# Optimization experiments

Measured on AMD Instinct MI355X. Metric: run time of the kernel, lower is better.

The kernel has to match this reference:

```python
import jax, jax.numpy as jnp
import numpy as np

EPS = 1e-5

def _ln(x, g, b):
    mu = jnp.mean(x, axis=-1, keepdims=True)
    var = jnp.mean(jnp.square(x - mu), axis=-1, keepdims=True)
    return (x - mu) * jax.lax.rsqrt(var + EPS) * g + b

def _lrelu(x):
    return jnp.where(x >= 0, x, 0.1 * x)  # LeakyReLU(0.1)

def _layer(x, w, b, g, be, act):
    # PointLinearLayer: Linear -> LayerNorm -> (optional) LeakyReLU(0.1)
    y = _ln(jnp.matmul(x, w) + b, g, be)
    return _lrelu(y) if act else y

def setup_inputs():
    key = jax.random.key(0)
    ks = jax.random.split(key, 16)
    B, Ns, Nd, K, Cin, Cout, PE, M = 1, 10000, 40000, 16, 128, 128, 32, 16
    w = lambda k, i, o: jax.random.normal(k, (i, o), jnp.float32) * 0.02
    z = lambda n: jnp.zeros((n,), jnp.float32)
    o = lambda n: jnp.ones((n,), jnp.float32)
    return {
        "sparse_xyz": jax.random.normal(ks[0], (B, Ns, 3), jnp.float32),
        "sparse_feats": jax.random.normal(ks[1], (B, Ns, Cin), jnp.float32),
        "nei_inds": jax.random.randint(ks[2], (B, Nd, K), 0, Ns),
        "sparse_xyz_norm": jax.random.normal(ks[3], (B, Ns, 3), jnp.float32),
        "dense_xyz": jax.random.normal(ks[4], (B, Nd, 3), jnp.float32),
        "dense_xyz_norm": jax.random.normal(ks[5], (B, Nd, 3), jnp.float32),
        "dense_feats": jax.random.normal(ks[6], (B, Nd, Cout), jnp.float32),
        # pe_convs WeightNet(3 -> 32, hidden=[32]): L0 3->32 LN+act, L1 32->32 LN
        "pe_w0": w(ks[7], 3, PE), "pe_b0": z(PE), "pe_g0": o(PE), "pe_be0": z(PE),
        "pe_w1": w(ks[8], PE, PE), "pe_b1": z(PE), "pe_g1": o(PE), "pe_be1": z(PE),
        # main WeightNet(3 -> 16, hidden=[16,16]): L0,L1 LN+act, L2 LN
        "wn_w0": w(ks[9], 3, M), "wn_b0": z(M), "wn_g0": o(M), "wn_be0": z(M),
        "wn_w1": w(ks[10], M, M), "wn_b1": z(M), "wn_g1": o(M), "wn_be1": z(M),
        "wn_w2": w(ks[11], M, M), "wn_b2": z(M), "wn_g2": o(M), "wn_be2": z(M),
        # final PointLinearLayer: (Cin+PE)*M -> Cout with LN + LeakyReLU(0.1)
        "lin_w": w(ks[12], (Cin + PE) * M, Cout), "lin_b": z(Cout),
        "lin_g": o(Cout), "lin_be": z(Cout),
    }

def reference(sparse_xyz, sparse_feats, nei_inds, sparse_xyz_norm, dense_xyz,
              dense_xyz_norm, dense_feats,
              pe_w0, pe_b0, pe_g0, pe_be0, pe_w1, pe_b1, pe_g1, pe_be1,
              wn_w0, wn_b0, wn_g0, wn_be0, wn_w1, wn_b1, wn_g1, wn_be1,
              wn_w2, wn_b2, wn_g2, wn_be2, lin_w, lin_b, lin_g, lin_be):
    gather = jax.vmap(lambda t, i: t[i])  # per-batch kNN gather
    loc = gather(sparse_xyz, nei_inds) - dense_xyz[:, :, None, :]   # B,Nd,K,3 relative coords (weightNetInput, USE_VI=False)
    g_feat = gather(sparse_feats, nei_inds)                          # B,Nd,K,Cin
    # positional-encoding WeightNet on relative coords (USE_PE)
    pe = _layer(loc, pe_w0, pe_b0, pe_g0, pe_be0, True)
    pe = _layer(pe, pe_w1, pe_b1, pe_g1, pe_be1, False)              # B,Nd,K,32
    feat = jnp.concatenate([g_feat, pe], axis=-1)                    # B,Nd,K,Cin+32
    # main WeightNet generates per-neighbor mixing weights
    wts = _layer(loc, wn_w0, wn_b0, wn_g0, wn_be0, True)
    wts = _layer(wts, wn_w1, wn_b1, wn_g1, wn_be1, True)
    wts = _layer(wts, wn_w2, wn_b2, wn_g2, wn_be2, False)            # B,Nd,K,16
    B, Nd = nei_inds.shape[:2]
    # matmul(feat^T, wts) over K, flatten channel x mid dims (C-major, matches torch .view)
    out = jnp.einsum('bnkc,bnkm->bncm', feat, wts).reshape(B, Nd, -1)
    out = _layer(out, lin_w, lin_b, lin_g, lin_be, True)             # B,Nd,Cout
    return out + dense_feats                                         # shortcut dense features
```

## Files before the change

kernel.cpp:

```cpp
#include <hip/hip_runtime.h>

#define NPB  16
#define KNN  16
#define CIN  128
#define CF   160
#define MM   16
#define PEC  32
#define COUT 128
#define KDIM 2560
#define FRE  768
#define LEPS 1e-5f

typedef __bf16 bf16x8 __attribute__((ext_vector_type(8)));
typedef float  f32x4  __attribute__((ext_vector_type(4)));
union U16x8 { uint4 u4; bf16x8 b; unsigned short us[8]; };

#define SW_PE_W0   0
#define SW_PE_B0   96
#define SW_PE_G0   128
#define SW_PE_BE0  160
#define SW_PE_W1   192
#define SW_PE_B1   1216
#define SW_PE_G1   1248
#define SW_PE_BE1  1280
#define SW_WN_W0   1312
#define SW_WN_B0   1360
#define SW_WN_G0   1376
#define SW_WN_BE0  1392
#define SW_WN_W1   1408
#define SW_WN_B1   1664
#define SW_WN_G1   1680
#define SW_WN_BE1  1696
#define SW_WN_W2   1712
#define SW_WN_B2   1968
#define SW_WN_G2   1984
#define SW_WN_BE2  2000
#define SW_TOTAL   2016

__device__ __forceinline__ float bf2f(unsigned short b){
  union { unsigned int u; float f; } x; x.u = ((unsigned int)b) << 16; return x.f;
}
__device__ __forceinline__ unsigned short f2bf(float f){
  union { float f; unsigned int u; } x; x.f = f;
  unsigned int r = (x.u + 0x7fffu + ((x.u >> 16) & 1u)) >> 16;
  return (unsigned short)r;
}
__device__ __forceinline__ unsigned short f2b(float f){
  union { __bf16 h; unsigned short u; } v; v.h = (__bf16)f; return v.u;
}
__device__ __forceinline__ float rsum16(float v){
  v += __shfl_xor(v, 8, 16);
  v += __shfl_xor(v, 4, 16);
  v += __shfl_xor(v, 2, 16);
  v += __shfl_xor(v, 1, 16);
  return v;
}
__device__ __forceinline__ float rsum32(float v){
  v += __shfl_xor(v, 16, 32);
  v += __shfl_xor(v, 8, 32);
  v += __shfl_xor(v, 4, 32);
  v += __shfl_xor(v, 2, 32);
  v += __shfl_xor(v, 1, 32);
  return v;
}
__device__ __forceinline__ float lrelu(float v){ return v >= 0.f ? v : 0.1f * v; }

template<int N>
__device__ __forceinline__ void ln_inlane(float* v, const float* g, const float* be, bool act){
  float mu = 0.f;
#pragma unroll
  for (int i = 0; i < N; ++i) mu += v[i];
  mu *= (1.f / N);
  float var = 0.f;
#pragma unroll
  for (int i = 0; i < N; ++i) { float d = v[i] - mu; var += d * d; }
  const float rs = rsqrtf(var * (1.f / N) + LEPS);
#pragma unroll
  for (int i = 0; i < N; ++i) {
    float y = (v[i] - mu) * rs * g[i] + be[i];
    v[i] = act ? lrelu(y) : y;
  }
}

__global__ __launch_bounds__(256)
void pct_prep(const float* __restrict__ lin_w, unsigned short* __restrict__ wpack,
              const float* __restrict__ sf, unsigned short* __restrict__ sfb16,
              const int n4)
{
  const int bid = blockIdx.x;
  if (bid < 160) {
    const int u    = bid * 256 + threadIdx.x;
    const int lane = u & 63;
    const int tt   = (u >> 6) & 7;
    const int s    = u >> 9;
    const int ipb  = s * 32 + ((lane >> 4) * 8);
    const int nn   = tt * 16 + (lane & 15);
    unsigned short v[8];
#pragma unroll
    for (int j = 0; j < 8; ++j) {
      const int ip  = ipb + j;
      const int r   = ip & 3;
      const int ctl = (ip >> 2) & 1;
      const int qq  = (ip >> 3) & 3;
      const int c16 = (ip >> 5) & 15;
      const int P   = ip >> 9;
      const int c   = P * 32 + ctl * 16 + c16;
      const int m   = qq * 4 + r;
      v[j] = f2bf(lin_w[(long)(c * MM + m) * COUT + nn]);
    }
    *(uint4*)(wpack + (long)u * 8) = *(uint4*)v;
  } else {
    const int i = (bid - 160) * 256 + threadIdx.x;
    if (i >= n4) return;
    const float4 v = ((const float4*)sf)[i];
    union { unsigned short us[4]; uint2 u; } r;
    r.us[0] = f2b(v.x); r.us[1] = f2b(v.y); r.us[2] = f2b(v.z); r.us[3] = f2b(v.w);
    ((uint2*)sfb16)[i] = r.u;
  }
}

__global__ __launch_bounds__(256)
void pct_nets(
    const float* __restrict__ sparse_xyz,
    const int* __restrict__ nei_inds,
    const float* __restrict__ dense_xyz,
    const float* __restrict__ pe_w0, const float* __restrict__ pe_b0,
    const float* __restrict__ pe_g0, const float* __restrict__ pe_be0,
    const float* __restrict__ pe_w1, const float* __restrict__ pe_b1,
    const float* __restrict__ pe_g1, const float* __restrict__ pe_be1,
    const float* __restrict__ wn_w0, const float* __restrict__ wn_b0,
    const float* __restrict__ wn_g0, const float* __restrict__ wn_be0,
    const float* __restrict__ wn_w1, const float* __restrict__ wn_b1,
    const float* __restrict__ wn_g1, const float* __restrict__ wn_be1,
    const float* __restrict__ wn_w2, const float* __restrict__ wn_b2,
    const float* __restrict__ wn_g2, const float* __restrict__ wn_be2,
    unsigned short* __restrict__ fragw)
{
  __shared__ float sw[SW_TOTAL];
  __shared__ __align__(16) unsigned short wtsf[16 * 256];
  __shared__ __align__(16) unsigned short pef[16 * 512];

  const int t     = threadIdx.x;
  const int nbase = blockIdx.x * NPB;

  for (int i = t; i < 96;   i += 256) sw[SW_PE_W0 + i] = pe_w0[i];
  for (int i = t; i < 32;   i += 256) {
    sw[SW_PE_B0 + i] = pe_b0[i];  sw[SW_PE_G0 + i] = pe_g0[i];  sw[SW_PE_BE0 + i] = pe_be0[i];
    sw[SW_PE_B1 + i] = pe_b1[i];  sw[SW_PE_G1 + i] = pe_g1[i];  sw[SW_PE_BE1 + i] = pe_be1[i];
  }
  for (int i = t; i < 1024; i += 256) sw[SW_PE_W1 + i] = pe_w1[i];
  for (int i = t; i < 48;   i += 256) sw[SW_WN_W0 + i] = wn_w0[i];
  for (int i = t; i < 16;   i += 256) {
    sw[SW_WN_B0 + i] = wn_b0[i];  sw[SW_WN_G0 + i] = wn_g0[i];  sw[SW_WN_BE0 + i] = wn_be0[i];
    sw[SW_WN_B1 + i] = wn_b1[i];  sw[SW_WN_G1 + i] = wn_g1[i];  sw[SW_WN_BE1 + i] = wn_be1[i];
    sw[SW_WN_B2 + i] = wn_b2[i];  sw[SW_WN_G2 + i] = wn_g2[i];  sw[SW_WN_BE2 + i] = wn_be2[i];
  }
  for (int i = t; i < 256;  i += 256) { sw[SW_WN_W1 + i] = wn_w1[i]; sw[SW_WN_W2 + i] = wn_w2[i]; }
  __syncthreads();

  {
    const int p  = t >> 4;
    const int kk = t & 15;
    const int n  = nbase + p;
    const int idx = nei_inds[n * KNN + kk];
    const float x0 = sparse_xyz[idx*3+0] - dense_xyz[n*3+0];
    const float x1 = sparse_xyz[idx*3+1] - dense_xyz[n*3+1];
    const float x2 = sparse_xyz[idx*3+2] - dense_xyz[n*3+2];

    float h[32];
#pragma unroll
    for (int c = 0; c < 32; ++c)
      h[c] = x0*sw[SW_PE_W0+c] + x1*sw[SW_PE_W0+32+c] + x2*sw[SW_PE_W0+64+c] + sw[SW_PE_B0+c];
    ln_inlane<32>(h, &sw[SW_PE_G0], &sw[SW_PE_BE0], true);

    float z[32];
#pragma unroll
    for (int c = 0; c < 32; ++c) z[c] = sw[SW_PE_B1 + c];
#pragma unroll 4
    for (int j = 0; j < 32; ++j) {
      const float hj = h[j];
#pragma unroll
      for (int c = 0; c < 32; ++c) z[c] += hj * sw[SW_PE_W1 + j*32 + c];
    }
    ln_inlane<32>(z, &sw[SW_PE_G1], &sw[SW_PE_BE1], false);
    {
      union { unsigned short us[32]; uint4 u4[4]; } zb;
#pragma unroll
      for (int c = 0; c < 32; ++c) zb.us[c] = f2b(z[c]);
      unsigned short* pp_ = pef + p*512 + kk*32;
#pragma unroll
      for (int j = 0; j < 4; ++j) *(uint4*)(pp_ + j*8) = zb.u4[j];
    }

    float w[16];
#pragma unroll
    for (int m = 0; m < 16; ++m)
      w[m] = x0*sw[SW_WN_W0+m] + x1*sw[SW_WN_W0+16+m] + x2*sw[SW_WN_W0+32+m] + sw[SW_WN_B0+m];
    ln_inlane<16>(w, &sw[SW_WN_G0], &sw[SW_WN_BE0], true);

    float z2[16];
#pragma unroll
    for (int m = 0; m < 16; ++m) z2[m] = sw[SW_WN_B1 + m];
#pragma unroll 4
    for (int j = 0; j < 16; ++j) {
      const float wj = w[j];
#pragma unroll
      for (int m = 0; m < 16; ++m) z2[m] += wj * sw[SW_WN_W1 + j*16 + m];
    }
    ln_inlane<16>(z2, &sw[SW_WN_G1], &sw[SW_WN_BE1], true);

#pragma unroll
    for (int m = 0; m < 16; ++m) w[m] = sw[SW_WN_B2 + m];
#pragma unroll 4
    for (int j = 0; j < 16; ++j) {
      const float wj = z2[j];
#pragma unroll
      for (int m = 0; m < 16; ++m) w[m] += wj * sw[SW_WN_W2 + j*16 + m];
    }
    ln_inlane<16>(w, &sw[SW_WN_G2], &sw[SW_WN_BE2], false);
    {
      unsigned short* wf = wtsf + p*256 + ((kk >> 3) << 7) + (kk & 7);
#pragma unroll
      for (int m = 0; m < 16; ++m) wf[m*8] = f2b(w[m]);
    }
  }

  {
    const int lane = t & 63;
    const int wave = t >> 6;
    const int l2   = lane & 31;
    const int ct2  = lane >> 5;
#pragma unroll
    for (int i = 0; i < 4; ++i) {
      const int p = wave*4 + i;
      unsigned short* fw = fragw + (size_t)(nbase + p) * FRE;
      if (lane < 32) {
        const uint4 a = *(const uint4*)(wtsf + p*256 + lane*8);
        *(uint4*)(fw + lane*8) = a;
      }
      union { unsigned short us[8]; uint4 u4; } o;
#pragma unroll
      for (int j = 0; j < 8; ++j)
        o.us[j] = pef[p*512 + ((l2 >> 4)*8 + j)*32 + ct2*16 + (l2 & 15)];
      *(uint4*)(fw + 256 + ct2*256 + l2*8) = o.u4;
    }
  }
}

__global__ __launch_bounds__(256)
void pct_eg(
    const int* __restrict__ nei_inds,
    const unsigned short* __restrict__ sfb16,
    const unsigned short* __restrict__ fragw,
    const unsigned short* __restrict__ wpack,
    const float* __restrict__ lin_b, const float* __restrict__ lin_g,
    const float* __restrict__ lin_be, const float* __restrict__ dense_feats,
    float* __restrict__ out)
{
  __shared__ __align__(16) union FU {
    unsigned short feats[16][2048];
    float outs[16][132];
  } fu;
  __shared__ __align__(16) unsigned short aL[16][512];

  const int t     = threadIdx.x;
  const int nbase = blockIdx.x * NPB;
  const int lane  = t & 63;
  const int wave  = t >> 6;
  const int q     = lane >> 4;
  const int mq    = lane & 15;

  int idxall[4][4];
#pragma unroll
  for (int i = 0; i < 4; ++i)
#pragma unroll
    for (int t4 = 0; t4 < 4; ++t4)
      idxall[i][t4] = nei_inds[(nbase + wave*4 + i) * KNN + t4*4 + q];

  U16x8 af[4], pe0[4], pe1[4];
  const uint4 zero4 = {0u, 0u, 0u, 0u};
#pragma unroll
  for (int i = 0; i < 4; ++i) {
    const int p = wave*4 + i;
#pragma unroll
    for (int t4 = 0; t4 < 4; ++t4)
      __builtin_amdgcn_global_load_lds(
          (const void*)(sfb16 + (size_t)idxall[i][t4] * CIN + mq * 8),
          (void*)((char*)fu.feats[p] + t4 * 1024), 16, 0, 0);
    const unsigned short* fw = fragw + (size_t)(nbase + p) * FRE;
    af[i].u4  = (lane < 32) ? *(const uint4*)(fw + lane*8) : zero4;
    pe0[i].u4 = *(const uint4*)(fw + 256 + (lane & 31)*8);
    pe1[i].u4 = *(const uint4*)(fw + 512 + (lane & 31)*8);
  }
  __syncthreads();

  f32x4 acc0 = {0.f,0.f,0.f,0.f}, acc1 = {0.f,0.f,0.f,0.f};
  const unsigned short* wpl = wpack + ((size_t)(wave*2) * 64 + lane) * 8;

#pragma unroll 1
  for (int P = 0; P < 5; ++P) {
#pragma unroll
    for (int i = 0; i < 4; ++i) {
      const int p = wave*4 + i;
      f32x4 a0 = {0.f,0.f,0.f,0.f}, a1 = {0.f,0.f,0.f,0.f};
      if (P < 4) {
        const unsigned short* sb = &fu.feats[p][0] + (q & 1) * 1024 + mq;
        U16x8 b0_, b1_;
#pragma unroll
        for (int j = 0; j < 8; ++j) b0_.us[j] = sb[j * CIN + (2*P    ) * 16];
#pragma unroll
        for (int j = 0; j < 8; ++j) b1_.us[j] = sb[j * CIN + (2*P + 1) * 16];
        a0 = __builtin_amdgcn_mfma_f32_16x16x32_bf16(af[i].b, b0_.b, a0, 0, 0, 0);
        a1 = __builtin_amdgcn_mfma_f32_16x16x32_bf16(af[i].b, b1_.b, a1, 0, 0, 0);
      } else {
        a0 = __builtin_amdgcn_mfma_f32_16x16x32_bf16(af[i].b, pe0[i].b, a0, 0, 0, 0);
        a1 = __builtin_amdgcn_mfma_f32_16x16x32_bf16(af[i].b, pe1[i].b, a1, 0, 0, 0);
      }
      union { unsigned short us[8]; uint4 u4; } o;
#pragma unroll
      for (int r = 0; r < 4; ++r) { o.us[r] = f2b(a0[r]); o.us[4+r] = f2b(a1[r]); }
      *(uint4*)((char*)aL[p] + ((mq*64 + q*16) ^ ((p & 7) << 4))) = o.u4;
    }
    __syncthreads();

#pragma unroll
    for (int s = 0; s < 16; ++s) {
      const int sg = P*16 + s;
      U16x8 af2;
      af2.u4 = *(const uint4*)((char*)aL[mq] + ((s*64 + q*16) ^ ((mq & 7) << 4)));
      const unsigned short* wpb = wpl + (size_t)sg * 4096;
      U16x8 b0_, b1_;
      b0_.u4 = *(const uint4*)(wpb);
      b1_.u4 = *(const uint4*)(wpb + 512);
      acc0 = __builtin_amdgcn_mfma_f32_16x16x32_bf16(af2.b, b0_.b, acc0, 0, 0, 0);
      acc1 = __builtin_amdgcn_mfma_f32_16x16x32_bf16(af2.b, b1_.b, acc1, 0, 0, 0);
    }
    __syncthreads();
  }

#pragma unroll
  for (int r = 0; r < 4; ++r) {
    fu.outs[q*4 + r][(wave*2    )*16 + mq] = acc0[r];
    fu.outs[q*4 + r][(wave*2 + 1)*16 + mq] = acc1[r];
  }
  __syncthreads();

  {
    const int p   = t >> 4;
    const int l16 = t & 15;
    const int n   = nbase + p;
    float v[8];
#pragma unroll
    for (int i = 0; i < 2; ++i) {
      const int cb = (i*16 + l16) * 4;
      const float4 r  = *(const float4*)(&fu.outs[p][cb]);
      const float4 bb = *(const float4*)(lin_b + cb);
      v[i*4+0] = r.x + bb.x; v[i*4+1] = r.y + bb.y;
      v[i*4+2] = r.z + bb.z; v[i*4+3] = r.w + bb.w;
    }
    float sum = 0.f;
#pragma unroll
    for (int i = 0; i < 8; ++i) sum += v[i];
    const float mu = rsum16(sum) * (1.f/128.f);
    float qs = 0.f;
#pragma unroll
    for (int i = 0; i < 8; ++i) { float d = v[i] - mu; qs += d*d; }
    const float rs = rsqrtf(rsum16(qs) * (1.f/128.f) + LEPS);
#pragma unroll
    for (int i = 0; i < 2; ++i) {
      const int cb = (i*16 + l16) * 4;
      const float4 g  = *(const float4*)(lin_g  + cb);
      const float4 be = *(const float4*)(lin_be + cb);
      const float4 df = *(const float4*)(dense_feats + (long)n*COUT + cb);
      float4 y;
      y.x = lrelu((v[i*4+0]-mu)*rs*g.x + be.x) + df.x;
      y.y = lrelu((v[i*4+1]-mu)*rs*g.y + be.y) + df.y;
      y.z = lrelu((v[i*4+2]-mu)*rs*g.z + be.z) + df.z;
      y.w = lrelu((v[i*4+3]-mu)*rs*g.w + be.w) + df.w;
      *(float4*)(out + (long)n*COUT + cb) = y;
    }
  }
}

__global__ __launch_bounds__(256)
void pct_fused(
    const float* __restrict__ sparse_xyz,
    const float* __restrict__ sparse_feats,
    const int* __restrict__ nei_inds,
    const float* __restrict__ dense_xyz,
    const float* __restrict__ dense_feats,
    const float* __restrict__ pe_w0, const float* __restrict__ pe_b0,
    const float* __restrict__ pe_g0, const float* __restrict__ pe_be0,
    const float* __restrict__ pe_w1, const float* __restrict__ pe_b1,
    const float* __restrict__ pe_g1, const float* __restrict__ pe_be1,
    const float* __restrict__ wn_w0, const float* __restrict__ wn_b0,
    const float* __restrict__ wn_g0, const float* __restrict__ wn_be0,
    const float* __restrict__ wn_w1, const float* __restrict__ wn_b1,
    const float* __restrict__ wn_g1, const float* __restrict__ wn_be1,
    const float* __restrict__ wn_w2, const float* __restrict__ wn_b2,
    const float* __restrict__ wn_g2, const float* __restrict__ wn_be2,
    const float* __restrict__ lin_w, const float* __restrict__ lin_b,
    const float* __restrict__ lin_g, const float* __restrict__ lin_be,
    float* __restrict__ out)
{
  __shared__ __align__(16) unsigned short feat_s[KNN][CF];
  __shared__ float wts_s[KNN][MM];
  __shared__ float loc_s[KNN][3];
  __shared__ int   nei_s[KNN];
  __shared__ __align__(16) unsigned short out_tile[CF*MM][8];

  const int t  = threadIdx.x;
  const int n0 = blockIdx.x * 8;
  const int k  = t >> 4;
  const int l  = t & 15;

#pragma unroll 1
  for (int p = 0; p < 8; ++p) {
    const int n = n0 + p;
    if (t < KNN) {
      int idx = nei_inds[n*KNN + t];
      nei_s[t] = idx;
      loc_s[t][0] = sparse_xyz[idx*3+0] - dense_xyz[n*3+0];
      loc_s[t][1] = sparse_xyz[idx*3+1] - dense_xyz[n*3+1];
      loc_s[t][2] = sparse_xyz[idx*3+2] - dense_xyz[n*3+2];
    }
    __syncthreads();
    {
      const int gk = t >> 4;
      const int c8 = (t & 15) * 8;
      const float* src = sparse_feats + (long)nei_s[gk]*CIN + c8;
      const float4 va = *(const float4*)(src);
      const float4 vb = *(const float4*)(src + 4);
      unsigned short* dst = &feat_s[gk][c8];
      dst[0] = f2bf(va.x); dst[1] = f2bf(va.y); dst[2] = f2bf(va.z); dst[3] = f2bf(va.w);
      dst[4] = f2bf(vb.x); dst[5] = f2bf(vb.y); dst[6] = f2bf(vb.z); dst[7] = f2bf(vb.w);
    }
    const float x0 = loc_s[k][0], x1 = loc_s[k][1], x2 = loc_s[k][2];
    const int c0 = l, c1 = l + 16;
    float ha = x0*pe_w0[0*PEC+c0] + x1*pe_w0[1*PEC+c0] + x2*pe_w0[2*PEC+c0] + pe_b0[c0];
    float hb = x0*pe_w0[0*PEC+c1] + x1*pe_w0[1*PEC+c1] + x2*pe_w0[2*PEC+c1] + pe_b0[c1];
    {
      float mu = rsum16(ha + hb) * (1.f/32.f);
      float da = ha - mu, db = hb - mu;
      float q  = rsum16(da*da + db*db);
      float rs = rsqrtf(q*(1.f/32.f) + LEPS);
      ha = lrelu(da*rs*pe_g0[c0] + pe_be0[c0]);
      hb = lrelu(db*rs*pe_g0[c1] + pe_be0[c1]);
    }
    float za = pe_b1[c0], zb = pe_b1[c1];
#pragma unroll
    for (int j = 0; j < 16; ++j) {
      float va = __shfl(ha, j, 16);
      float vb = __shfl(hb, j, 16);
      za += va * pe_w1[j*PEC + c0] + vb * pe_w1[(j+16)*PEC + c0];
      zb += va * pe_w1[j*PEC + c1] + vb * pe_w1[(j+16)*PEC + c1];
    }
    {
      float mu = rsum16(za + zb) * (1.f/32.f);
      float da = za - mu, db = zb - mu;
      float q  = rsum16(da*da + db*db);
      float rs = rsqrtf(q*(1.f/32.f) + LEPS);
      feat_s[k][CIN + c0] = f2bf(da*rs*pe_g1[c0] + pe_be1[c0]);
      feat_s[k][CIN + c1] = f2bf(db*rs*pe_g1[c1] + pe_be1[c1]);
    }
    float w0v = x0*wn_w0[0*MM+l] + x1*wn_w0[1*MM+l] + x2*wn_w0[2*MM+l] + wn_b0[l];
    {
      float mu = rsum16(w0v) * (1.f/16.f);
      float d  = w0v - mu;
      float rs = rsqrtf(rsum16(d*d)*(1.f/16.f) + LEPS);
      w0v = lrelu(d*rs*wn_g0[l] + wn_be0[l]);
    }
    float w1v = wn_b1[l];
#pragma unroll
    for (int j = 0; j < 16; ++j)
      w1v += __shfl(w0v, j, 16) * wn_w1[j*MM + l];
    {
      float mu = rsum16(w1v) * (1.f/16.f);
      float d  = w1v - mu;
      float rs = rsqrtf(rsum16(d*d)*(1.f/16.f) + LEPS);
      w1v = lrelu(d*rs*wn_g1[l] + wn_be1[l]);
    }
    float w2v = wn_b2[l];
#pragma unroll
    for (int j = 0; j < 16; ++j)
      w2v += __shfl(w1v, j, 16) * wn_w2[j*MM + l];
    {
      float mu = rsum16(w2v) * (1.f/16.f);
      float d  = w2v - mu;
      float rs = rsqrtf(rsum16(d*d)*(1.f/16.f) + LEPS);
      w2v = d*rs*wn_g2[l] + wn_be2[l];
    }
    wts_s[k][l] = w2v;
    __syncthreads();
    {
      const int m = t & 15;
      const int g = t >> 4;
      float wv[KNN];
#pragma unroll
      for (int kk = 0; kk < KNN; ++kk) wv[kk] = wts_s[kk][m];
#pragma unroll
      for (int j = 0; j < 10; ++j) {
        const int c = g*10 + j;
        float acc = 0.f;
#pragma unroll
        for (int kk = 0; kk < KNN; ++kk)
          acc += bf2f(feat_s[kk][c]) * wv[kk];
        out_tile[c*MM + m][p] = f2bf(acc);
      }
    }
    __syncthreads();
  }
  {
    const int h  = t >> 6;
    const int o0 = (t & 63) * 2;
    float acc0[8], acc1[8];
#pragma unroll
    for (int p = 0; p < 8; ++p) { acc0[p] = 0.f; acc1[p] = 0.f; }
    const int i0 = h * 640;
    for (int i = i0; i < i0 + 640; ++i) {
      const float2 wv = *(const float2*)(lin_w + (long)i*COUT + o0);
      const float wa = wv.x;
      const float wc = wv.y;
      const uint4 r = *(const uint4*)(&out_tile[i][0]);
      const float f0 = bf2f((unsigned short)(r.x & 0xffffu));
      const float f1 = bf2f((unsigned short)(r.x >> 16));
      const float g2 = bf2f((unsigned short)(r.y & 0xffffu));
      const float g3 = bf2f((unsigned short)(r.y >> 16));
      const float g4 = bf2f((unsigned short)(r.z & 0xffffu));
      const float g5 = bf2f((unsigned short)(r.z >> 16));
      const float g6 = bf2f((unsigned short)(r.w & 0xffffu));
      const float g7 = bf2f((unsigned short)(r.w >> 16));
      acc0[0] += f0*wa; acc1[0] += f0*wc;
      acc0[1] += f1*wa; acc1[1] += f1*wc;
      acc0[2] += g2*wa; acc1[2] += g2*wc;
      acc0[3] += g3*wa; acc1[3] += g3*wc;
      acc0[4] += g4*wa; acc1[4] += g4*wc;
      acc0[5] += g5*wa; acc1[5] += g5*wc;
      acc0[6] += g6*wa; acc1[6] += g6*wc;
      acc0[7] += g7*wa; acc1[7] += g7*wc;
    }
    __syncthreads();
    float* red = (float*)&out_tile[0][0];
#pragma unroll
    for (int p = 0; p < 8; ++p) {
      red[((h*8 + p) << 7) + o0    ] = acc0[p];
      red[((h*8 + p) << 7) + o0 + 1] = acc1[p];
    }
    __syncthreads();
    const int p2 = t >> 5, l2 = t & 31;
    const int n  = n0 + p2;
    float v[4];
#pragma unroll
    for (int j = 0; j < 4; ++j) {
      const int o = l2 + (j << 5);
      float sv = red[((0*8 + p2) << 7) + o] + red[((1*8 + p2) << 7) + o]
               + red[((2*8 + p2) << 7) + o] + red[((3*8 + p2) << 7) + o];
      v[j] = sv + lin_b[o];
    }
    float mu = rsum32(v[0] + v[1] + v[2] + v[3]) * (1.f/128.f);
    float q = 0.f;
#pragma unroll
    for (int j = 0; j < 4; ++j) { float d = v[j] - mu; q += d*d; }
    float rs = rsqrtf(rsum32(q) * (1.f/128.f) + LEPS);
#pragma unroll
    for (int j = 0; j < 4; ++j) {
      const int o = l2 + (j << 5);
      float y = (v[j] - mu) * rs * lin_g[o] + lin_be[o];
      y = lrelu(y);
      y += dense_feats[n*COUT + o];
      out[n*COUT + o] = y;
    }
  }
}

extern "C" void kernel_launch(void* const* d_in, const int* in_sizes, int n_in,
                              void* d_out, int out_size, void* d_ws, size_t ws_size,
                              hipStream_t stream) {
  const int Nd = in_sizes[2] / KNN;
  const int Ns = in_sizes[1] / CIN;
  const size_t fr_bytes = (size_t)Nd * FRE * 2;
  const size_t w_bytes  = (size_t)KDIM * COUT * 2;
  const size_t f_bytes  = (size_t)Ns * CIN * 2;
  const bool use_split = (ws_size >= fr_bytes + w_bytes + f_bytes)
                         && (Nd % NPB == 0) && ((Ns * CIN) % 4 == 0);

  if (use_split) {
    unsigned short* fragw = (unsigned short*)d_ws;
    unsigned short* wpack = (unsigned short*)((char*)d_ws + fr_bytes);
    unsigned short* sfb16 = (unsigned short*)((char*)d_ws + fr_bytes + w_bytes);

    const int n4 = Ns * CIN / 4;
    pct_prep<<<dim3(160 + (n4 + 255)/256), dim3(256), 0, stream>>>(
      (const float*)d_in[27], wpack, (const float*)d_in[1], sfb16, n4);

    pct_nets<<<dim3(Nd / NPB), dim3(256), 0, stream>>>(
      (const float*)d_in[0],  (const int*)d_in[2],  (const float*)d_in[4],
      (const float*)d_in[7],  (const float*)d_in[8],  (const float*)d_in[9],  (const float*)d_in[10],
      (const float*)d_in[11], (const float*)d_in[12], (const float*)d_in[13], (const float*)d_in[14],
      (const float*)d_in[15], (const float*)d_in[16], (const float*)d_in[17], (const float*)d_in[18],
      (const float*)d_in[19], (const float*)d_in[20], (const float*)d_in[21], (const float*)d_in[22],
      (const float*)d_in[23], (const float*)d_in[24], (const float*)d_in[25], (const float*)d_in[26],
      fragw);

    pct_eg<<<dim3(Nd / NPB), dim3(256), 0, stream>>>(
      (const int*)d_in[2], sfb16, fragw, wpack,
      (const float*)d_in[28], (const float*)d_in[29], (const float*)d_in[30],
      (const float*)d_in[6], (float*)d_out);
  } else {
    pct_fused<<<dim3(Nd / 8), dim3(256), 0, stream>>>(
      (const float*)d_in[0],  (const float*)d_in[1],  (const int*)d_in[2],
      (const float*)d_in[4],  (const float*)d_in[6],
      (const float*)d_in[7],  (const float*)d_in[8],  (const float*)d_in[9],  (const float*)d_in[10],
      (const float*)d_in[11], (const float*)d_in[12], (const float*)d_in[13], (const float*)d_in[14],
      (const float*)d_in[15], (const float*)d_in[16], (const float*)d_in[17], (const float*)d_in[18],
      (const float*)d_in[19], (const float*)d_in[20], (const float*)d_in[21], (const float*)d_in[22],
      (const float*)d_in[23], (const float*)d_in[24], (const float*)d_in[25], (const float*)d_in[26],
      (const float*)d_in[27], (const float*)d_in[28], (const float*)d_in[29], (const float*)d_in[30],
      (float*)d_out);
  }
}
```

Baseline: 284.1 us.

## Split gather-GEMM kernel across 8 waves and swizzle feature LDS layout

Doubles the block to 512 threads so each wave handles two points and a single 16-column output tile of the final linear layer. This halves per-wave register state and weight streaming. It also XOR-swizzles the gathered neighbor-feature rows in LDS so the strided column reads avoid bank conflicts. The epilogue LayerNorm is remapped to 32 threads per point. The cost is more waves contending for barriers and the same per-block LDS footprint.

After: 318.7 us. +12.2%, slower.

```diff
diff --git a/kernel.cpp b/kernel.cpp
--- a/kernel.cpp
+++ b/kernel.cpp
@@ -247,7 +247,7 @@
   }
 }
 
-__global__ __launch_bounds__(256)
+__global__ __launch_bounds__(512, 4)
 void pct_eg(
     const int* __restrict__ nei_inds,
     const unsigned short* __restrict__ sfb16,
@@ -269,23 +269,26 @@
   const int wave  = t >> 6;
   const int q     = lane >> 4;
   const int mq    = lane & 15;
-
-  int idxall[4][4];
-#pragma unroll
-  for (int i = 0; i < 4; ++i)
+  const int q1    = q & 1;
+  const int mqh   = mq >> 3, mql = mq & 7;
+
+  int idxall[2][4];
+#pragma unroll
+  for (int i = 0; i < 2; ++i)
 #pragma unroll
     for (int t4 = 0; t4 < 4; ++t4)
-      idxall[i][t4] = nei_inds[(nbase + wave*4 + i) * KNN + t4*4 + q];
-
-  U16x8 af[4], pe0[4], pe1[4];
+      idxall[i][t4] = nei_inds[(nbase + wave*2 + i) * KNN + t4*4 + q];
+
+  U16x8 af[2], pe0[2], pe1[2];
   const uint4 zero4 = {0u, 0u, 0u, 0u};
 #pragma unroll
-  for (int i = 0; i < 4; ++i) {
-    const int p = wave*4 + i;
+  for (int i = 0; i < 2; ++i) {
+    const int p = wave*2 + i;
 #pragma unroll
     for (int t4 = 0; t4 < 4; ++t4)
       __builtin_amdgcn_global_load_lds(
-          (const void*)(sfb16 + (size_t)idxall[i][t4] * CIN + mq * 8),
+          (const void*)(sfb16 + (size_t)idxall[i][t4] * CIN
+                        + ((mq ^ ((t4 >> 1) << 1)) * 8)),
           (void*)((char*)fu.feats[p] + t4 * 1024), 16, 0, 0);
     const unsigned short* fw = fragw + (size_t)(nbase + p) * FRE;
     af[i].u4  = (lane < 32) ? *(const uint4*)(fw + lane*8) : zero4;
@@ -294,22 +297,23 @@
   }
   __syncthreads();
 
-  f32x4 acc0 = {0.f,0.f,0.f,0.f}, acc1 = {0.f,0.f,0.f,0.f};
-  const unsigned short* wpl = wpack + ((size_t)(wave*2) * 64 + lane) * 8;
+  f32x4 acc = {0.f,0.f,0.f,0.f};
 
 #pragma unroll 1
   for (int P = 0; P < 5; ++P) {
 #pragma unroll
-    for (int i = 0; i < 4; ++i) {
-      const int p = wave*4 + i;
+    for (int i = 0; i < 2; ++i) {
+      const int p = wave*2 + i;
       f32x4 a0 = {0.f,0.f,0.f,0.f}, a1 = {0.f,0.f,0.f,0.f};
       if (P < 4) {
-        const unsigned short* sb = &fu.feats[p][0] + (q & 1) * 1024 + mq;
+        const int slot0 = (4*P     + mqh) ^ (q1 << 1);
+        const int slot1 = (4*P + 2 + mqh) ^ (q1 << 1);
+        const unsigned short* fb = &fu.feats[p][0] + q1*1024 + mql;
         U16x8 b0_, b1_;
 #pragma unroll
-        for (int j = 0; j < 8; ++j) b0_.us[j] = sb[j * CIN + (2*P    ) * 16];
-#pragma unroll
-        for (int j = 0; j < 8; ++j) b1_.us[j] = sb[j * CIN + (2*P + 1) * 16];
+        for (int j = 0; j < 8; ++j) b0_.us[j] = fb[j*128 + slot0*8];
+#pragma unroll
+        for (int j = 0; j < 8; ++j) b1_.us[j] = fb[j*128 + slot1*8];
         a0 = __builtin_amdgcn_mfma_f32_16x16x32_bf16(af[i].b, b0_.b, a0, 0, 0, 0);
         a1 = __builtin_amdgcn_mfma_f32_16x16x32_bf16(af[i].b, b1_.b, a1, 0, 0, 0);
       } else {
@@ -328,57 +332,40 @@
       const int sg = P*16 + s;
       U16x8 af2;
       af2.u4 = *(const uint4*)((char*)aL[mq] + ((s*64 + q*16) ^ ((mq & 7) << 4)));
-      const unsigned short* wpb = wpl + (size_t)sg * 4096;
-      U16x8 b0_, b1_;
-      b0_.u4 = *(const uint4*)(wpb);
-      b1_.u4 = *(const uint4*)(wpb + 512);
-      acc0 = __builtin_amdgcn_mfma_f32_16x16x32_bf16(af2.b, b0_.b, acc0, 0, 0, 0);
-      acc1 = __builtin_amdgcn_mfma_f32_16x16x32_bf16(af2.b, b1_.b, acc1, 0, 0, 0);
+      U16x8 b_;
+      b_.u4 = *(const uint4*)(wpack + ((size_t)(sg*8 + wave) * 64 + lane) * 8);
+      acc = __builtin_amdgcn_mfma_f32_16x16x32_bf16(af2.b, b_.b, acc, 0, 0, 0);
     }
     __syncthreads();
   }
 
 #pragma unroll
-  for (int r = 0; r < 4; ++r) {
-    fu.outs[q*4 + r][(wave*2    )*16 + mq] = acc0[r];
-    fu.outs[q*4 + r][(wave*2 + 1)*16 + mq] = acc1[r];
-  }
+  for (int r = 0; r < 4; ++r)
+    fu.outs[q*4 + r][wave*16 + mq] = acc[r];
   __syncthreads();
 
   {
-    const int p   = t >> 4;
-    const int l16 = t & 15;
+    const int p   = t >> 5;
+    const int l32 = t & 31;
     const int n   = nbase + p;
-    float v[8];
-#pragma unroll
-    for (int i = 0; i < 2; ++i) {
-      const int cb = (i*16 + l16) * 4;
-      const float4 r  = *(const float4*)(&fu.outs[p][cb]);
-      const float4 bb = *(const float4*)(lin_b + cb);
-      v[i*4+0] = r.x + bb.x; v[i*4+1] = r.y + bb.y;
-      v[i*4+2] = r.z + bb.z; v[i*4+3] = r.w + bb.w;
-    }
-    float sum = 0.f;
-#pragma unroll
-    for (int i = 0; i < 8; ++i) sum += v[i];
-    const float mu = rsum16(sum) * (1.f/128.f);
+    const int cb  = l32 * 4;
+    const float4 r  = *(const float4*)(&fu.outs[p][cb]);
+    const float4 bb = *(const float4*)(lin_b + cb);
+    float v[4] = { r.x + bb.x, r.y + bb.y, r.z + bb.z, r.w + bb.w };
+    const float mu = rsum32(v[0] + v[1] + v[2] + v[3]) * (1.f/128.f);
     float qs = 0.f;
 #pragma unroll
-    for (int i = 0; i < 8; ++i) { float d = v[i] - mu; qs += d*d; }
-    const float rs = rsqrtf(rsum16(qs) * (1.f/128.f) + LEPS);
-#pragma unroll
-    for (int i = 0; i < 2; ++i) {
-      const int cb = (i*16 + l16) * 4;
-      const float4 g  = *(const float4*)(lin_g  + cb);
-      const float4 be = *(const float4*)(lin_be + cb);
-      const float4 df = *(const float4*)(dense_feats + (long)n*COUT + cb);
-      float4 y;
-      y.x = lrelu((v[i*4+0]-mu)*rs*g.x + be.x) + df.x;
-      y.y = lrelu((v[i*4+1]-mu)*rs*g.y + be.y) + df.y;
-      y.z = lrelu((v[i*4+2]-mu)*rs*g.z + be.z) + df.z;
-      y.w = lrelu((v[i*4+3]-mu)*rs*g.w + be.w) + df.w;
-      *(float4*)(out + (long)n*COUT + cb) = y;
-    }
+    for (int i = 0; i < 4; ++i) { float d = v[i] - mu; qs += d*d; }
+    const float rs = rsqrtf(rsum32(qs) * (1.f/128.f) + LEPS);
+    const float4 g  = *(const float4*)(lin_g  + cb);
+    const float4 be = *(const float4*)(lin_be + cb);
+    const float4 df = *(const float4*)(dense_feats + (long)n*COUT + cb);
+    float4 y;
+    y.x = lrelu((v[0]-mu)*rs*g.x + be.x) + df.x;
+    y.y = lrelu((v[1]-mu)*rs*g.y + be.y) + df.y;
+    y.z = lrelu((v[2]-mu)*rs*g.z + be.z) + df.z;
+    y.w = lrelu((v[3]-mu)*rs*g.w + be.w) + df.w;
+    *(float4*)(out + (long)n*COUT + cb) = y;
   }
 }
 
@@ -602,7 +589,7 @@
       (const float*)d_in[23], (const float*)d_in[24], (const float*)d_in[25], (const float*)d_in[26],
       fragw);
 
-    pct_eg<<<dim3(Nd / NPB), dim3(256), 0, stream>>>(
+    pct_eg<<<dim3(Nd / NPB), dim3(512), 0, stream>>>(
       (const int*)d_in[2], sfb16, fragw, wpack,
       (const float*)d_in[28], (const float*)d_in[29], (const float*)d_in[30],
       (const float*)d_in[6], (float*)d_out);
```

## Fuse weight-net kernel into gather-MFMA kernel, dropping fragw global round trip

Applied to the files above, without the earlier changes.

Merges pct_nets and pct_eg into a single pct_all kernel. The PE and weight-net MLP outputs now stay in registers and a shared-memory union instead of being written to a global fragw buffer and read back. The feature gather also gets an XOR-swizzled LDS layout, intended to cut bank conflicts on the B-fragment reads. This saves one launch and about 61 MB of global traffic, at the cost of a longer per-block critical path and a union that overlaps the net scratch with the feats buffer, which needs the barrier placed correctly.

New measurement: 337.0 us. +18.6%, slower.

```diff
diff --git a/kernel.cpp b/kernel.cpp
--- a/kernel.cpp
+++ b/kernel.cpp
@@ -8,7 +8,6 @@
 #define PEC  32
 #define COUT 128
 #define KDIM 2560
-#define FRE  768
 #define LEPS 1e-5f
 
 typedef __bf16 bf16x8 __attribute__((ext_vector_type(8)));
@@ -120,10 +119,11 @@
 }
 
 __global__ __launch_bounds__(256)
-void pct_nets(
+void pct_all(
     const float* __restrict__ sparse_xyz,
     const int* __restrict__ nei_inds,
     const float* __restrict__ dense_xyz,
+    const unsigned short* __restrict__ sfb16,
     const float* __restrict__ pe_w0, const float* __restrict__ pe_b0,
     const float* __restrict__ pe_g0, const float* __restrict__ pe_be0,
     const float* __restrict__ pe_w1, const float* __restrict__ pe_b1,
@@ -134,15 +134,39 @@
     const float* __restrict__ wn_g1, const float* __restrict__ wn_be1,
     const float* __restrict__ wn_w2, const float* __restrict__ wn_b2,
     const float* __restrict__ wn_g2, const float* __restrict__ wn_be2,
-    unsigned short* __restrict__ fragw)
+    const unsigned short* __restrict__ wpack,
+    const float* __restrict__ lin_b, const float* __restrict__ lin_g,
+    const float* __restrict__ lin_be, const float* __restrict__ dense_feats,
+    float* __restrict__ out)
 {
-  __shared__ float sw[SW_TOTAL];
-  __shared__ __align__(16) unsigned short wtsf[16 * 256];
-  __shared__ __align__(16) unsigned short pef[16 * 512];
+  __shared__ __align__(16) union FU {
+    struct {
+      float sw[SW_TOTAL];
+      unsigned short wtsf[16 * 256];
+      unsigned short pef[16 * 512];
+    } n;
+    unsigned short feats[16][2048];
+    float outs[16][132];
+  } fu;
+  __shared__ __align__(16) unsigned short aL[16][512];
 
   const int t     = threadIdx.x;
   const int nbase = blockIdx.x * NPB;
-
+  const int lane  = t & 63;
+  const int wave  = t >> 6;
+  const int q     = lane >> 4;
+  const int mq    = lane & 15;
+  const int q1    = q & 1;
+  const int mqh   = mq >> 3, mql = mq & 7;
+
+  int idxall[4][4];
+#pragma unroll
+  for (int i = 0; i < 4; ++i)
+#pragma unroll
+    for (int t4 = 0; t4 < 4; ++t4)
+      idxall[i][t4] = nei_inds[(nbase + wave*4 + i) * KNN + t4*4 + q];
+
+  float* sw = fu.n.sw;
   for (int i = t; i < 96;   i += 256) sw[SW_PE_W0 + i] = pe_w0[i];
   for (int i = t; i < 32;   i += 256) {
     sw[SW_PE_B0 + i] = pe_b0[i];  sw[SW_PE_G0 + i] = pe_g0[i];  sw[SW_PE_BE0 + i] = pe_be0[i];
@@ -187,7 +211,7 @@
       union { unsigned short us[32]; uint4 u4[4]; } zb;
 #pragma unroll
       for (int c = 0; c < 32; ++c) zb.us[c] = f2b(z[c]);
-      unsigned short* pp_ = pef + p*512 + kk*32;
+      unsigned short* pp_ = fu.n.pef + p*512 + kk*32;
 #pragma unroll
       for (int j = 0; j < 4; ++j) *(uint4*)(pp_ + j*8) = zb.u4[j];
     }
@@ -219,78 +243,41 @@
     }
     ln_inlane<16>(w, &sw[SW_WN_G2], &sw[SW_WN_BE2], false);
     {
-      unsigned short* wf = wtsf + p*256 + ((kk >> 3) << 7) + (kk & 7);
+      unsigned short* wf = fu.n.wtsf + p*256 + ((kk >> 3) << 7) + (kk & 7);
 #pragma unroll
       for (int m = 0; m < 16; ++m) wf[m*8] = f2b(w[m]);
     }
   }
 
+  U16x8 af[4], pe0[4], pe1[4];
+  const uint4 zero4 = {0u, 0u, 0u, 0u};
   {
-    const int lane = t & 63;
-    const int wave = t >> 6;
-    const int l2   = lane & 31;
-    const int ct2  = lane >> 5;
+    const int l2 = lane & 31;
 #pragma unroll
     for (int i = 0; i < 4; ++i) {
       const int p = wave*4 + i;
-      unsigned short* fw = fragw + (size_t)(nbase + p) * FRE;
-      if (lane < 32) {
-        const uint4 a = *(const uint4*)(wtsf + p*256 + lane*8);
-        *(uint4*)(fw + lane*8) = a;
+      af[i].u4 = (lane < 32) ? *(const uint4*)(fu.n.wtsf + p*256 + lane*8) : zero4;
+      U16x8 e0, e1;
+#pragma unroll
+      for (int j = 0; j < 8; ++j) {
+        const int ro = p*512 + ((l2 >> 4)*8 + j)*32 + (l2 & 15);
+        e0.us[j] = fu.n.pef[ro];
+        e1.us[j] = fu.n.pef[ro + 16];
       }
-      union { unsigned short us[8]; uint4 u4; } o;
-#pragma unroll
-      for (int j = 0; j < 8; ++j)
-        o.us[j] = pef[p*512 + ((l2 >> 4)*8 + j)*32 + ct2*16 + (l2 & 15)];
-      *(uint4*)(fw + 256 + ct2*256 + l2*8) = o.u4;
-    }
-  }
-}
-
-__global__ __launch_bounds__(256)
-void pct_eg(
-    const int* __restrict__ nei_inds,
-    const unsigned short* __restrict__ sfb16,
-    const unsigned short* __restrict__ fragw,
-    const unsigned short* __restrict__ wpack,
-    const float* __restrict__ lin_b, const float* __restrict__ lin_g,
-    const float* __restrict__ lin_be, const float* __restrict__ dense_feats,
-    float* __restrict__ out)
-{
-  __shared__ __align__(16) union FU {
-    unsigned short feats[16][2048];
-    float outs[16][132];
-  } fu;
-  __shared__ __align__(16) unsigned short aL[16][512];
-
-  const int t     = threadIdx.x;
-  const int nbase = blockIdx.x * NPB;
-  const int lane  = t & 63;
-  const int wave  = t >> 6;
-  const int q     = lane >> 4;
-  const int mq    = lane & 15;
-
-  int idxall[4][4];
-#pragma unroll
-  for (int i = 0; i < 4; ++i)
-#pragma unroll
-    for (int t4 = 0; t4 < 4; ++t4)
-      idxall[i][t4] = nei_inds[(nbase + wave*4 + i) * KNN + t4*4 + q];
-
-  U16x8 af[4], pe0[4], pe1[4];
-  const uint4 zero4 = {0u, 0u, 0u, 0u};
+      pe0[i] = e0; pe1[i] = e1;
+    }
+  }
+  __syncthreads();
+
 #pragma unroll
   for (int i = 0; i < 4; ++i) {
     const int p = wave*4 + i;
 #pragma unroll
     for (int t4 = 0; t4 < 4; ++t4)
       __builtin_amdgcn_global_load_lds(
-          (const void*)(sfb16 + (size_t)idxall[i][t4] * CIN + mq * 8),
+          (const void*)(sfb16 + (size_t)idxall[i][t4] * CIN
+                        + ((mq ^ ((t4 >> 1) << 1)) * 8)),
           (void*)((char*)fu.feats[p] + t4 * 1024), 16, 0, 0);
-    const unsigned short* fw = fragw + (size_t)(nbase + p) * FRE;
-    af[i].u4  = (lane < 32) ? *(const uint4*)(fw + lane*8) : zero4;
-    pe0[i].u4 = *(const uint4*)(fw + 256 + (lane & 31)*8);
-    pe1[i].u4 = *(const uint4*)(fw + 512 + (lane & 31)*8);
   }
   __syncthreads();
 
@@ -304,12 +291,14 @@
       const int p = wave*4 + i;
       f32x4 a0 = {0.f,0.f,0.f,0.f}, a1 = {0.f,0.f,0.f,0.f};
       if (P < 4) {
-        const unsigned short* sb = &fu.feats[p][0] + (q & 1) * 1024 + mq;
+        const int slot0 = (4*P     + mqh) ^ (q1 << 1);
+        const int slot1 = (4*P + 2 + mqh) ^ (q1 << 1);
+        const unsigned short* fb = &fu.feats[p][0] + q1*1024 + mql;
         U16x8 b0_, b1_;
 #pragma unroll
-        for (int j = 0; j < 8; ++j) b0_.us[j] = sb[j * CIN + (2*P    ) * 16];
-#pragma unroll
-        for (int j = 0; j < 8; ++j) b1_.us[j] = sb[j * CIN + (2*P + 1) * 16];
+        for (int j = 0; j < 8; ++j) b0_.us[j] = fb[j*128 + slot0*8];
+#pragma unroll
+        for (int j = 0; j < 8; ++j) b1_.us[j] = fb[j*128 + slot1*8];
         a0 = __builtin_amdgcn_mfma_f32_16x16x32_bf16(af[i].b, b0_.b, a0, 0, 0, 0);
         a1 = __builtin_amdgcn_mfma_f32_16x16x32_bf16(af[i].b, b1_.b, a1, 0, 0, 0);
       } else {
@@ -578,32 +567,28 @@
                               hipStream_t stream) {
   const int Nd = in_sizes[2] / KNN;
   const int Ns = in_sizes[1] / CIN;
-  const size_t fr_bytes = (size_t)Nd * FRE * 2;
-  const size_t w_bytes  = (size_t)KDIM * COUT * 2;
-  const size_t f_bytes  = (size_t)Ns * CIN * 2;
-  const bool use_split = (ws_size >= fr_bytes + w_bytes + f_bytes)
+  const size_t w_bytes = (size_t)KDIM * COUT * 2;
+  const size_t f_bytes = (size_t)Ns * CIN * 2;
+  const bool use_split = (ws_size >= w_bytes + f_bytes)
                          && (Nd % NPB == 0) && ((Ns * CIN) % 4 == 0);
 
   if (use_split) {
-    unsigned short* fragw = (unsigned short*)d_ws;
-    unsigned short* wpack = (unsigned short*)((char*)d_ws + fr_bytes);
-    unsigned short* sfb16 = (unsigned short*)((char*)d_ws + fr_bytes + w_bytes);
+    unsigned short* wpack = (unsigned short*)d_ws;
+    unsigned short* sfb16 = (unsigned short*)((char*)d_ws + w_bytes);
 
     const int n4 = Ns * CIN / 4;
     pct_prep<<<dim3(160 + (n4 + 255)/256), dim3(256), 0, stream>>>(
       (const float*)d_in[27], wpack, (const float*)d_in[1], sfb16, n4);
 
-    pct_nets<<<dim3(Nd / NPB), dim3(256), 0, stream>>>(
+    pct_all<<<dim3(Nd / NPB), dim3(256), 0, stream>>>(
       (const float*)d_in[0],  (const int*)d_in[2],  (const float*)d_in[4],
+      sfb16,
       (const float*)d_in[7],  (const float*)d_in[8],  (const float*)d_in[9],  (const float*)d_in[10],
       (const float*)d_in[11], (const float*)d_in[12], (const float*)d_in[13], (const float*)d_in[14],
       (const float*)d_in[15], (const float*)d_in[16], (const float*)d_in[17], (const float*)d_in[18],
       (const float*)d_in[19], (const float*)d_in[20], (const float*)d_in[21], (const float*)d_in[22],
       (const float*)d_in[23], (const float*)d_in[24], (const float*)d_in[25], (const float*)d_in[26],
-      fragw);
-
-    pct_eg<<<dim3(Nd / NPB), dim3(256), 0, stream>>>(
-      (const int*)d_in[2], sfb16, fragw, wpack,
+      wpack,
       (const float*)d_in[28], (const float*)d_in[29], (const float*)d_in[30],
       (const float*)d_in[6], (float*)d_out);
   } else {
```

## Compute PE second layer with bf16 MFMA instead of scalar FMA loops

Applied to the files above, without the earlier changes.

Moves the 32x32 positional-encoding linear layer from per-lane scalar FMAs over shared-memory weights onto MFMA 16x16x32 bf16 instructions. The prep kernel pre-packs pe_w1 into MFMA B-fragment layout, each wave stages per-point hidden activations in shared memory, and LayerNorm is done with 16-lane shuffle reductions. This removes about 1K FMAs per thread and the LDS weight reads, at the cost of bf16 rounding of the hidden activations and weights, extra LDS staging, and a serial loop over four points per wave.

Result: no change. 284.0 us (median of 2 runs) (-0.0%).

```diff
diff --git a/kernel.cpp b/kernel.cpp
--- a/kernel.cpp
+++ b/kernel.cpp
@@ -19,23 +19,22 @@
 #define SW_PE_B0   96
 #define SW_PE_G0   128
 #define SW_PE_BE0  160
-#define SW_PE_W1   192
-#define SW_PE_B1   1216
-#define SW_PE_G1   1248
-#define SW_PE_BE1  1280
-#define SW_WN_W0   1312
-#define SW_WN_B0   1360
-#define SW_WN_G0   1376
-#define SW_WN_BE0  1392
-#define SW_WN_W1   1408
-#define SW_WN_B1   1664
-#define SW_WN_G1   1680
-#define SW_WN_BE1  1696
-#define SW_WN_W2   1712
-#define SW_WN_B2   1968
-#define SW_WN_G2   1984
-#define SW_WN_BE2  2000
-#define SW_TOTAL   2016
+#define SW_PE_B1   192
+#define SW_PE_G1   224
+#define SW_PE_BE1  256
+#define SW_WN_W0   288
+#define SW_WN_B0   336
+#define SW_WN_G0   352
+#define SW_WN_BE0  368
+#define SW_WN_W1   384
+#define SW_WN_B1   640
+#define SW_WN_G1   656
+#define SW_WN_BE1  672
+#define SW_WN_W2   688
+#define SW_WN_B2   944
+#define SW_WN_G2   960
+#define SW_WN_BE2  976
+#define SW_TOTAL   992
 
 __device__ __forceinline__ float bf2f(unsigned short b){
   union { unsigned int u; float f; } x; x.u = ((unsigned int)b) << 16; return x.f;
@@ -84,6 +83,7 @@
 
 __global__ __launch_bounds__(256)
 void pct_prep(const float* __restrict__ lin_w, unsigned short* __restrict__ wpack,
+              const float* __restrict__ pe_w1, unsigned short* __restrict__ w1f,
               const float* __restrict__ sf, unsigned short* __restrict__ sfb16,
               const int n4)
 {
@@ -109,8 +109,19 @@
       v[j] = f2bf(lin_w[(long)(c * MM + m) * COUT + nn]);
     }
     *(uint4*)(wpack + (long)u * 8) = *(uint4*)v;
+  } else if (bid == 160) {
+    const int u = threadIdx.x;
+    if (u < 128) {
+      const int ct = u >> 6;
+      const int l  = u & 63;
+      unsigned short v[8];
+#pragma unroll
+      for (int e = 0; e < 8; ++e)
+        v[e] = f2bf(pe_w1[((l >> 4) * 8 + e) * 32 + ct * 16 + (l & 15)]);
+      *(uint4*)(w1f + (ct * 64 + l) * 8) = *(uint4*)v;
+    }
   } else {
-    const int i = (bid - 160) * 256 + threadIdx.x;
+    const int i = (bid - 161) * 256 + threadIdx.x;
     if (i >= n4) return;
     const float4 v = ((const float4*)sf)[i];
     union { unsigned short us[4]; uint2 u; } r;
@@ -126,7 +137,7 @@
     const float* __restrict__ dense_xyz,
     const float* __restrict__ pe_w0, const float* __restrict__ pe_b0,
     const float* __restrict__ pe_g0, const float* __restrict__ pe_be0,
-    const float* __restrict__ pe_w1, const float* __restrict__ pe_b1,
+    const unsigned short* __restrict__ w1f, const float* __restrict__ pe_b1,
     const float* __restrict__ pe_g1, const float* __restrict__ pe_be1,
     const float* __restrict__ wn_w0, const float* __restrict__ wn_b0,
     const float* __restrict__ wn_g0, const float* __restrict__ wn_be0,
@@ -139,16 +150,18 @@
   __shared__ float sw[SW_TOTAL];
   __shared__ __align__(16) unsigned short wtsf[16 * 256];
   __shared__ __align__(16) unsigned short pef[16 * 512];
+  __shared__ __align__(16) unsigned short hstage[4][16 * 40];
 
   const int t     = threadIdx.x;
   const int nbase = blockIdx.x * NPB;
+  const int lane  = t & 63;
+  const int wave  = t >> 6;
 
   for (int i = t; i < 96;   i += 256) sw[SW_PE_W0 + i] = pe_w0[i];
   for (int i = t; i < 32;   i += 256) {
     sw[SW_PE_B0 + i] = pe_b0[i];  sw[SW_PE_G0 + i] = pe_g0[i];  sw[SW_PE_BE0 + i] = pe_be0[i];
     sw[SW_PE_B1 + i] = pe_b1[i];  sw[SW_PE_G1 + i] = pe_g1[i];  sw[SW_PE_BE1 + i] = pe_be1[i];
   }
-  for (int i = t; i < 1024; i += 256) sw[SW_PE_W1 + i] = pe_w1[i];
   for (int i = t; i < 48;   i += 256) sw[SW_WN_W0 + i] = wn_w0[i];
   for (int i = t; i < 16;   i += 256) {
     sw[SW_WN_B0 + i] = wn_b0[i];  sw[SW_WN_G0 + i] = wn_g0[i];  sw[SW_WN_BE0 + i] = wn_be0[i];
@@ -156,11 +169,15 @@
     sw[SW_WN_B2 + i] = wn_b2[i];  sw[SW_WN_G2 + i] = wn_g2[i];  sw[SW_WN_BE2 + i] = wn_be2[i];
   }
   for (int i = t; i < 256;  i += 256) { sw[SW_WN_W1 + i] = wn_w1[i]; sw[SW_WN_W2 + i] = wn_w2[i]; }
+
+  U16x8 w1b0, w1b1;
+  w1b0.u4 = *(const uint4*)(w1f + lane * 8);
+  w1b1.u4 = *(const uint4*)(w1f + 512 + lane * 8);
   __syncthreads();
 
+  const int p  = t >> 4;
+  const int kk = t & 15;
   {
-    const int p  = t >> 4;
-    const int kk = t & 15;
     const int n  = nbase + p;
     const int idx = nei_inds[n * KNN + kk];
     const float x0 = sparse_xyz[idx*3+0] - dense_xyz[n*3+0];
@@ -173,23 +190,43 @@
       h[c] = x0*sw[SW_PE_W0+c] + x1*sw[SW_PE_W0+32+c] + x2*sw[SW_PE_W0+64+c] + sw[SW_PE_B0+c];
     ln_inlane<32>(h, &sw[SW_PE_G0], &sw[SW_PE_BE0], true);
 
-    float z[32];
-#pragma unroll
-    for (int c = 0; c < 32; ++c) z[c] = sw[SW_PE_B1 + c];
-#pragma unroll 4
-    for (int j = 0; j < 32; ++j) {
-      const float hj = h[j];
-#pragma unroll
-      for (int c = 0; c < 32; ++c) z[c] += hj * sw[SW_PE_W1 + j*32 + c];
-    }
-    ln_inlane<32>(z, &sw[SW_PE_G1], &sw[SW_PE_BE1], false);
-    {
-      union { unsigned short us[32]; uint4 u4[4]; } zb;
-#pragma unroll
-      for (int c = 0; c < 32; ++c) zb.us[c] = f2b(z[c]);
-      unsigned short* pp_ = pef + p*512 + kk*32;
-#pragma unroll
-      for (int j = 0; j < 4; ++j) *(uint4*)(pp_ + j*8) = zb.u4[j];
+    union { unsigned short us[32]; uint4 u4[4]; } hb;
+#pragma unroll
+    for (int c = 0; c < 32; ++c) hb.us[c] = f2b(h[c]);
+
+    const float g0  = sw[SW_PE_G1 + (lane & 15)];
+    const float g1v = sw[SW_PE_G1 + 16 + (lane & 15)];
+    const float be0 = sw[SW_PE_BE1 + (lane & 15)];
+    const float be1 = sw[SW_PE_BE1 + 16 + (lane & 15)];
+    const float b1lo = sw[SW_PE_B1 + (lane & 15)];
+    const float b1hi = sw[SW_PE_B1 + 16 + (lane & 15)];
+    unsigned short* hs = &hstage[wave][0];
+
+#pragma unroll
+    for (int i = 0; i < 4; ++i) {
+      if ((p & 3) == i) {
+#pragma unroll
+        for (int c4 = 0; c4 < 4; ++c4)
+          *(uint4*)(hs + kk*40 + c4*8) = hb.u4[c4];
+      }
+      U16x8 ha_;
+      ha_.u4 = *(const uint4*)(hs + (lane & 15)*40 + (lane >> 4)*8);
+      f32x4 z0 = {0.f,0.f,0.f,0.f}, z1 = {0.f,0.f,0.f,0.f};
+      z0 = __builtin_amdgcn_mfma_f32_16x16x32_bf16(ha_.b, w1b0.b, z0, 0, 0, 0);
+      z1 = __builtin_amdgcn_mfma_f32_16x16x32_bf16(ha_.b, w1b1.b, z1, 0, 0, 0);
+      unsigned short* pp_ = pef + (wave*4 + i) * 512;
+#pragma unroll
+      for (int r = 0; r < 4; ++r) {
+        const float v0 = z0[r] + b1lo;
+        const float v1 = z1[r] + b1hi;
+        const float mu = rsum16(v0 + v1) * (1.f/32.f);
+        const float d0 = v0 - mu, d1 = v1 - mu;
+        const float qv = rsum16(d0*d0 + d1*d1);
+        const float rsv = rsqrtf(qv * (1.f/32.f) + LEPS);
+        const int krow = (lane >> 4)*4 + r;
+        pp_[krow*32 + (lane & 15)]      = f2b(d0*rsv*g0 + be0);
+        pp_[krow*32 + 16 + (lane & 15)] = f2b(d1*rsv*g1v + be1);
+      }
     }
 
     float w[16];
@@ -226,22 +263,20 @@
   }
 
   {
-    const int lane = t & 63;
-    const int wave = t >> 6;
     const int l2   = lane & 31;
     const int ct2  = lane >> 5;
 #pragma unroll
     for (int i = 0; i < 4; ++i) {
-      const int p = wave*4 + i;
-      unsigned short* fw = fragw + (size_t)(nbase + p) * FRE;
+      const int pp = wave*4 + i;
+      unsigned short* fw = fragw + (size_t)(nbase + pp) * FRE;
       if (lane < 32) {
-        const uint4 a = *(const uint4*)(wtsf + p*256 + lane*8);
+        const uint4 a = *(const uint4*)(wtsf + pp*256 + lane*8);
         *(uint4*)(fw + lane*8) = a;
       }
       union { unsigned short us[8]; uint4 u4; } o;
 #pragma unroll
       for (int j = 0; j < 8; ++j)
-        o.us[j] = pef[p*512 + ((l2 >> 4)*8 + j)*32 + ct2*16 + (l2 & 15)];
+        o.us[j] = pef[pp*512 + ((l2 >> 4)*8 + j)*32 + ct2*16 + (l2 & 15)];
       *(uint4*)(fw + 256 + ct2*256 + l2*8) = o.u4;
     }
   }
@@ -580,23 +615,26 @@
   const int Ns = in_sizes[1] / CIN;
   const size_t fr_bytes = (size_t)Nd * FRE * 2;
   const size_t w_bytes  = (size_t)KDIM * COUT * 2;
+  const size_t w1_bytes = 4096;
   const size_t f_bytes  = (size_t)Ns * CIN * 2;
-  const bool use_split = (ws_size >= fr_bytes + w_bytes + f_bytes)
+  const bool use_split = (ws_size >= fr_bytes + w_bytes + w1_bytes + f_bytes)
                          && (Nd % NPB == 0) && ((Ns * CIN) % 4 == 0);
 
   if (use_split) {
     unsigned short* fragw = (unsigned short*)d_ws;
     unsigned short* wpack = (unsigned short*)((char*)d_ws + fr_bytes);
-    unsigned short* sfb16 = (unsigned short*)((char*)d_ws + fr_bytes + w_bytes);
+    unsigned short* w1f   = (unsigned short*)((char*)d_ws + fr_bytes + w_bytes);
+    unsigned short* sfb16 = (unsigned short*)((char*)d_ws + fr_bytes + w_bytes + w1_bytes);
 
     const int n4 = Ns * CIN / 4;
-    pct_prep<<<dim3(160 + (n4 + 255)/256), dim3(256), 0, stream>>>(
-      (const float*)d_in[27], wpack, (const float*)d_in[1], sfb16, n4);
+    pct_prep<<<dim3(161 + (n4 + 255)/256), dim3(256), 0, stream>>>(
+      (const float*)d_in[27], wpack, (const float*)d_in[11], w1f,
+      (const float*)d_in[1], sfb16, n4);
 
     pct_nets<<<dim3(Nd / NPB), dim3(256), 0, stream>>>(
       (const float*)d_in[0],  (const int*)d_in[2],  (const float*)d_in[4],
       (const float*)d_in[7],  (const float*)d_in[8],  (const float*)d_in[9],  (const float*)d_in[10],
-      (const float*)d_in[11], (const float*)d_in[12], (const float*)d_in[13], (const float*)d_in[14],
+      w1f,                    (const float*)d_in[12], (const float*)d_in[13], (const float*)d_in[14],
       (const float*)d_in[15], (const float*)d_in[16], (const float*)d_in[17], (const float*)d_in[18],
       (const float*)d_in[19], (const float*)d_in[20], (const float*)d_in[21], (const float*)d_in[22],
       (const float*)d_in[23], (const float*)d_in[24], (const float*)d_in[25], (const float*)d_in[26],
```
